# Kernel tuning notes

Measured on AMD Instinct MI355X. Metric: run time of the kernel, lower is better.

The kernel has to match this reference:

```python
import jax, jax.numpy as jnp
import numpy as np

NX, NY = 1024, 512
LX, LY = 0.26, 0.12
NU = 1e-4
U_INLET = 0.1
DX = LX / (NX - 1)
DY = LY / (NY - 1)
W_CONT, W_MOM, W_BC = 1.0, 0.1, 1.0


def _pad_x(f):
    # replicate pad along x axis (dim -2)
    return jnp.pad(f, ((0, 0), (0, 0), (1, 1), (0, 0)), mode='edge')


def _pad_y(f):
    return jnp.pad(f, ((0, 0), (0, 0), (0, 0), (1, 1)), mode='edge')


def ddx(f):
    p = _pad_x(f)
    return (p[:, :, 2:, :] - p[:, :, :-2, :]) / (2.0 * DX)


def ddy(f):
    p = _pad_y(f)
    return (p[:, :, :, 2:] - p[:, :, :, :-2]) / (2.0 * DY)


def d2dx2(f):
    p = _pad_x(f)
    return (p[:, :, 2:, :] - 2.0 * f + p[:, :, :-2, :]) / (DX * DX)


def d2dy2(f):
    p = _pad_y(f)
    return (p[:, :, :, 2:] - 2.0 * f + p[:, :, :, :-2]) / (DY * DY)


def masked_mean(x, mask):
    return (x * mask).sum() / jnp.maximum(mask.sum(), 1.0)


def region_masks(x_in):
    r = x_in[:, 1:2].astype(jnp.float32)  # [B,1,NX,NY] region codes
    fluid = (r > 0.5).astype(jnp.float32)
    obstacle = (r < 0.5).astype(jnp.float32)
    wall = ((r > 1.5) & (r < 2.5)).astype(jnp.float32)
    inlet = ((r > 2.5) & (r < 3.5)).astype(jnp.float32)
    outlet = (r > 3.5).astype(jnp.float32)
    noslip = ((obstacle + wall) > 0.5).astype(jnp.float32)
    # interior = fluid with zeroed 1-cell border
    border = jnp.zeros((NX, NY), jnp.float32).at[1:-1, 1:-1].set(1.0)
    interior = fluid * border
    return fluid, interior, noslip, inlet, outlet


def setup_inputs() -> dict:
    key = jax.random.key(0)
    k1, k2 = jax.random.split(key)
    y_hat = jax.random.normal(k1, (16, 3, NX, NY), dtype=jnp.float32)
    x_in = jax.random.randint(k2, (16, 2, NX, NY), 0, 5).astype(jnp.int32)
    return {'y_hat': y_hat, 'x_in': x_in}


def reference(y_hat, x_in):
    ux = y_hat[:, 0:1]
    uy = y_hat[:, 1:2]
    p = y_hat[:, 2:3]
    fluid, interior, noslip, inlet, outlet = region_masks(x_in)

    # continuity
    div = ddx(ux) + ddy(uy)
    l_cont = masked_mean(div ** 2, interior)

    # momentum
    res_x = ux * ddx(ux) + uy * ddy(ux) + ddx(p) - NU * (d2dx2(ux) + d2dy2(ux))
    res_y = ux * ddx(uy) + uy * ddy(uy) + ddy(p) - NU * (d2dx2(uy) + d2dy2(uy))
    l_mom = masked_mean(res_x ** 2, interior) + masked_mean(res_y ** 2, interior)

    # boundary (masked_mean already returns 0 for empty masks via denom clamp)
    l_bc = masked_mean(ux ** 2, noslip) + masked_mean(uy ** 2, noslip)
    l_bc = l_bc + masked_mean((ux - U_INLET) ** 2, inlet) + masked_mean(uy ** 2, inlet)
    l_bc = l_bc + masked_mean(ddx(ux) ** 2, outlet)

    total = W_CONT * l_cont + W_MOM * l_mom + W_BC * l_bc
    return jnp.stack([l_cont, l_mom, l_bc, total])
```

## Files before the change

kernel.cpp:

```cpp
#include <hip/hip_runtime.h>


namespace {
constexpr int NXc  = 1024;
constexpr int NYc  = 512;
constexpr int NXYc = NXc * NYc;
constexpr int NBc  = 16;
constexpr int NTHR = 256;
constexpr int NACC = 10;
constexpr int TR   = 4;
constexpr int NCH  = NXc / TR;
constexpr int NBLK = NBc * NCH;
constexpr int NXCD = 8;
constexpr int QX   = NBLK / NXCD;
}

__global__ __launch_bounds__(NTHR) void pil_main(const float* __restrict__ y,
                                                 const int* __restrict__ xin,
                                                 float* __restrict__ partial) {
  constexpr double DXd = 0.26 / 1023.0;
  constexpr double DYd = 0.12 / 511.0;
  const float INV2DX = (float)(1.0 / (2.0 * DXd));
  const float INV2DY = (float)(1.0 / (2.0 * DYd));
  const float INVDX2 = (float)(1.0 / (DXd * DXd));
  const float INVDY2 = (float)(1.0 / (DYd * DYd));
  constexpr float NU = 1e-4f;
  constexpr float U_INLET = 0.1f;

  __shared__ float lf[3][TR + 2][NYc];

  const int l   = threadIdx.x & 63;
  const int w   = threadIdx.x >> 6;
  const int swz = (blockIdx.x % NXCD) * QX + blockIdx.x / NXCD;
  const int b   = swz >> 8;
  const int i0  = (swz & (NCH - 1)) * TR;

  const float* __restrict__ ux = y + (size_t)b * 3 * NXYc;
  const float* __restrict__ uy = ux + NXYc;
  const float* __restrict__ pp = ux + 2 * NXYc;
  const int*   __restrict__ rp = xin + (size_t)(2 * b + 1) * NXYc;

#pragma unroll
  for (int k = 0; k < 9; ++k) {
    const int c  = k * 4 + w;
    const int f  = c / 12;
    const int cc = c % 12;
    const int rw = cc >> 1;
    const int h  = cc & 1;
    int gi = i0 - 1 + rw;
    gi = gi < 0 ? 0 : (gi > NXc - 1 ? NXc - 1 : gi);
    const float* base = (f == 0) ? ux : ((f == 1) ? uy : pp);
    const float* g = base + gi * NYc + h * 256 + l * 4;
    float* d = &lf[f][rw][h * 256];
    __builtin_amdgcn_global_load_lds(
        (const __attribute__((address_space(1))) void*)g,
        (__attribute__((address_space(3))) void*)d, 16, 0, 0);
  }

  const int i = i0 + w;
  const int jc = l << 3;
  const int4 R0 = *reinterpret_cast<const int4*>(rp + i * NYc + jc);
  const int4 R1 = *reinterpret_cast<const int4*>(rp + i * NYc + jc + 4);

  __syncthreads();

  const float4 Cxl = *reinterpret_cast<const float4*>(&lf[0][w + 1][jc]);
  const float4 Cxh = *reinterpret_cast<const float4*>(&lf[0][w + 1][jc + 4]);
  const float4 Cyl = *reinterpret_cast<const float4*>(&lf[1][w + 1][jc]);
  const float4 Cyh = *reinterpret_cast<const float4*>(&lf[1][w + 1][jc + 4]);
  const float4 Cpl = *reinterpret_cast<const float4*>(&lf[2][w + 1][jc]);
  const float4 Cph = *reinterpret_cast<const float4*>(&lf[2][w + 1][jc + 4]);
  const float4 Pxl = *reinterpret_cast<const float4*>(&lf[0][w][jc]);
  const float4 Pxh = *reinterpret_cast<const float4*>(&lf[0][w][jc + 4]);
  const float4 Pyl = *reinterpret_cast<const float4*>(&lf[1][w][jc]);
  const float4 Pyh = *reinterpret_cast<const float4*>(&lf[1][w][jc + 4]);
  const float4 Ppl = *reinterpret_cast<const float4*>(&lf[2][w][jc]);
  const float4 Pph = *reinterpret_cast<const float4*>(&lf[2][w][jc + 4]);
  const float4 Nxl = *reinterpret_cast<const float4*>(&lf[0][w + 2][jc]);
  const float4 Nxh = *reinterpret_cast<const float4*>(&lf[0][w + 2][jc + 4]);
  const float4 Nyl = *reinterpret_cast<const float4*>(&lf[1][w + 2][jc]);
  const float4 Nyh = *reinterpret_cast<const float4*>(&lf[1][w + 2][jc + 4]);
  const float4 Npl = *reinterpret_cast<const float4*>(&lf[2][w + 2][jc]);
  const float4 Nph = *reinterpret_cast<const float4*>(&lf[2][w + 2][jc + 4]);

  float a[NACC];
#pragma unroll
  for (int k = 0; k < NACC; ++k) a[k] = 0.f;

  const float cx[8]  = {Cxl.x, Cxl.y, Cxl.z, Cxl.w, Cxh.x, Cxh.y, Cxh.z, Cxh.w};
  const float cy_[8] = {Cyl.x, Cyl.y, Cyl.z, Cyl.w, Cyh.x, Cyh.y, Cyh.z, Cyh.w};
  const float cp_[8] = {Cpl.x, Cpl.y, Cpl.z, Cpl.w, Cph.x, Cph.y, Cph.z, Cph.w};
  const float pxA[8] = {Pxl.x, Pxl.y, Pxl.z, Pxl.w, Pxh.x, Pxh.y, Pxh.z, Pxh.w};
  const float pyA[8] = {Pyl.x, Pyl.y, Pyl.z, Pyl.w, Pyh.x, Pyh.y, Pyh.z, Pyh.w};
  const float ppA[8] = {Ppl.x, Ppl.y, Ppl.z, Ppl.w, Pph.x, Pph.y, Pph.z, Pph.w};
  const float nxA[8] = {Nxl.x, Nxl.y, Nxl.z, Nxl.w, Nxh.x, Nxh.y, Nxh.z, Nxh.w};
  const float nyA[8] = {Nyl.x, Nyl.y, Nyl.z, Nyl.w, Nyh.x, Nyh.y, Nyh.z, Nyh.w};
  const float npA[8] = {Npl.x, Npl.y, Npl.z, Npl.w, Nph.x, Nph.y, Nph.z, Nph.w};
  const int   rA[8]  = {R0.x, R0.y, R0.z, R0.w, R1.x, R1.y, R1.z, R1.w};

  float lxx = __shfl_up(cx[7], 1, 64);    if (l == 0)  lxx = cx[0];
  float rxx = __shfl_down(cx[0], 1, 64);  if (l == 63) rxx = cx[7];
  float lyy = __shfl_up(cy_[7], 1, 64);   if (l == 0)  lyy = cy_[0];
  float ryy = __shfl_down(cy_[0], 1, 64); if (l == 63) ryy = cy_[7];
  float lpp = __shfl_up(cp_[7], 1, 64);   if (l == 0)  lpp = cp_[0];
  float rpp = __shfl_down(cp_[0], 1, 64); if (l == 63) rpp = cp_[7];

  const bool irow = (i >= 1) & (i <= NXc - 2);

#pragma unroll
  for (int e = 0; e < 8; ++e) {
    const int   r    = rA[e];
    const float c_ux = cx[e], c_uy = cy_[e];
    const float uxm = (e == 0) ? lxx : cx[e - 1];
    const float uxp = (e == 7) ? rxx : cx[e + 1];
    const float uym = (e == 0) ? lyy : cy_[e - 1];
    const float uyp = (e == 7) ? ryy : cy_[e + 1];
    const float pm_ = (e == 0) ? lpp : cp_[e - 1];
    const float pq_ = (e == 7) ? rpp : cp_[e + 1];

    const float ddx_ux = (nxA[e] - pxA[e]) * INV2DX;
    const float ddy_ux = (uxp - uxm) * INV2DY;
    const float ddx_uy = (nyA[e] - pyA[e]) * INV2DX;
    const float ddy_uy = (uyp - uym) * INV2DY;

    const bool jedge = ((l == 0) & (e == 0)) | ((l == 63) & (e == 7));
    const bool interior = (r >= 1) & irow & (!jedge);
    if (interior) {
      const float dv    = ddx_ux + ddy_uy;
      const float d2xux = (nxA[e] - 2.f * c_ux + pxA[e]) * INVDX2;
      const float d2yux = (uxp - 2.f * c_ux + uxm) * INVDY2;
      const float d2xuy = (nyA[e] - 2.f * c_uy + pyA[e]) * INVDX2;
      const float d2yuy = (uyp - 2.f * c_uy + uym) * INVDY2;
      const float ddx_p = (npA[e] - ppA[e]) * INV2DX;
      const float ddy_p = (pq_ - pm_) * INV2DY;
      const float rxv = c_ux * ddx_ux + c_uy * ddy_ux + ddx_p - NU * (d2xux + d2yux);
      const float ryv = c_ux * ddx_uy + c_uy * ddy_uy + ddy_p - NU * (d2xuy + d2yuy);
      a[0] += dv * dv;
      a[1] += rxv * rxv;
      a[2] += ryv * ryv;
      a[3] += 1.f;
    }
    if ((r == 0) | (r == 2)) {
      a[4] += c_ux * c_ux + c_uy * c_uy;
      a[5] += 1.f;
    }
    if (r == 3) {
      const float d = c_ux - U_INLET;
      a[6] += d * d + c_uy * c_uy;
      a[7] += 1.f;
    }
    if (r == 4) {
      a[8] += ddx_ux * ddx_ux;
      a[9] += 1.f;
    }
  }

#pragma unroll
  for (int k = 0; k < NACC; ++k) {
    float v = a[k];
#pragma unroll
    for (int off = 32; off > 0; off >>= 1) v += __shfl_down(v, off, 64);
    a[k] = v;
  }

  __shared__ float sacc[NTHR / 64][NACC];
  if (l == 0) {
#pragma unroll
    for (int k = 0; k < NACC; ++k) sacc[w][k] = a[k];
  }
  __syncthreads();
  if (threadIdx.x < NACC) {
    float s = 0.f;
#pragma unroll
    for (int ww = 0; ww < NTHR / 64; ++ww) s += sacc[ww][threadIdx.x];
    partial[threadIdx.x * NBLK + blockIdx.x] = s;
  }
}

__global__ __launch_bounds__(256) void pil_finalize(const float* __restrict__ partial,
                                                    float* __restrict__ out) {
  __shared__ double sw[NACC][4];
  const int t = threadIdx.x;
  const int lane = t & 63, wave = t >> 6;
#pragma unroll
  for (int k = 0; k < NACC; ++k) {
    double v = 0.0;
    const float4* p4 = reinterpret_cast<const float4*>(partial + (size_t)k * NBLK);
    for (int bb = t; bb < NBLK / 4; bb += 256) {
      const float4 q = p4[bb];
      v += (double)q.x + (double)q.y + (double)q.z + (double)q.w;
    }
#pragma unroll
    for (int off = 32; off > 0; off >>= 1) v += __shfl_down(v, off, 64);
    if (lane == 0) sw[k][wave] = v;
  }
  __syncthreads();
  if (t == 0) {
    double acc[NACC];
#pragma unroll
    for (int k = 0; k < NACC; ++k) {
      double s = 0.0;
#pragma unroll
      for (int ww = 0; ww < 4; ++ww) s += sw[k][ww];
      acc[k] = s;
    }
    const double l_cont = acc[0] / fmax(acc[3], 1.0);
    const double l_mom  = (acc[1] + acc[2]) / fmax(acc[3], 1.0);
    const double l_bc   = acc[4] / fmax(acc[5], 1.0)
                        + acc[6] / fmax(acc[7], 1.0)
                        + acc[8] / fmax(acc[9], 1.0);
    const double total  = 1.0 * l_cont + 0.1 * l_mom + 1.0 * l_bc;
    out[0] = (float)l_cont;
    out[1] = (float)l_mom;
    out[2] = (float)l_bc;
    out[3] = (float)total;
  }
}

extern "C" void kernel_launch(void* const* d_in, const int* in_sizes, int n_in,
                              void* d_out, int out_size, void* d_ws, size_t ws_size,
                              hipStream_t stream) {
  const float* y   = (const float*)d_in[0];
  const int*   xin = (const int*)d_in[1];
  float* partial   = (float*)d_ws;

  pil_main<<<NBLK, NTHR, 0, stream>>>(y, xin, partial);
  pil_finalize<<<1, 256, 0, stream>>>(partial, (float*)d_out);
}
```

Measured before the change: 53.50 us.

## Double rows per block and load halo rows directly into registers

Each block now covers 8 rows with 512 threads instead of 4 rows with 256, which halves the number of blocks and lowers the share of redundant halo rows per block. The two halo rows are no longer staged in LDS. The first and last waves load them straight from global memory into registers, and the other waves read their neighbour rows from LDS. This cuts total global halo traffic and LDS footprint per row. The cost is larger blocks, divergent branches for the edge waves, and halo loads that are not covered by the async LDS copy.

```diff
diff --git a/kernel.cpp b/kernel.cpp
--- a/kernel.cpp
+++ b/kernel.cpp
@@ -6,9 +6,9 @@
 constexpr int NYc  = 512;
 constexpr int NXYc = NXc * NYc;
 constexpr int NBc  = 16;
-constexpr int NTHR = 256;
+constexpr int NTHR = 512;
 constexpr int NACC = 10;
-constexpr int TR   = 4;
+constexpr int TR   = 8;
 constexpr int NCH  = NXc / TR;
 constexpr int NBLK = NBc * NCH;
 constexpr int NXCD = 8;
@@ -27,12 +27,12 @@
   constexpr float NU = 1e-4f;
   constexpr float U_INLET = 0.1f;
 
-  __shared__ float lf[3][TR + 2][NYc];
+  __shared__ float lf[3][TR][NYc];
 
   const int l   = threadIdx.x & 63;
   const int w   = threadIdx.x >> 6;
   const int swz = (blockIdx.x % NXCD) * QX + blockIdx.x / NXCD;
-  const int b   = swz >> 8;
+  const int b   = swz >> 7;
   const int i0  = (swz & (NCH - 1)) * TR;
 
   const float* __restrict__ ux = y + (size_t)b * 3 * NXYc;
@@ -41,47 +41,69 @@
   const int*   __restrict__ rp = xin + (size_t)(2 * b + 1) * NXYc;
 
 #pragma unroll
-  for (int k = 0; k < 9; ++k) {
-    const int c  = k * 4 + w;
-    const int f  = c / 12;
-    const int cc = c % 12;
+  for (int k = 0; k < 6; ++k) {
+    const int c  = k * 8 + w;
+    const int f  = c >> 4;
+    const int cc = c & 15;
     const int rw = cc >> 1;
     const int h  = cc & 1;
-    int gi = i0 - 1 + rw;
-    gi = gi < 0 ? 0 : (gi > NXc - 1 ? NXc - 1 : gi);
     const float* base = (f == 0) ? ux : ((f == 1) ? uy : pp);
-    const float* g = base + gi * NYc + h * 256 + l * 4;
+    const float* g = base + (i0 + rw) * NYc + h * 256 + l * 4;
     float* d = &lf[f][rw][h * 256];
     __builtin_amdgcn_global_load_lds(
         (const __attribute__((address_space(1))) void*)g,
         (__attribute__((address_space(3))) void*)d, 16, 0, 0);
   }
 
-  const int i = i0 + w;
+  const int i  = i0 + w;
   const int jc = l << 3;
+
   const int4 R0 = *reinterpret_cast<const int4*>(rp + i * NYc + jc);
   const int4 R1 = *reinterpret_cast<const int4*>(rp + i * NYc + jc + 4);
 
+  float4 Hxl = {}, Hxh = {}, Hyl = {}, Hyh = {}, Hpl = {}, Hph = {};
+  if ((w == 0) | (w == 7)) {
+    const int hr = (w == 0) ? (i0 > 0 ? i0 - 1 : 0)
+                            : (i0 + TR < NXc ? i0 + TR : NXc - 1);
+    Hxl = *reinterpret_cast<const float4*>(ux + hr * NYc + jc);
+    Hxh = *reinterpret_cast<const float4*>(ux + hr * NYc + jc + 4);
+    Hyl = *reinterpret_cast<const float4*>(uy + hr * NYc + jc);
+    Hyh = *reinterpret_cast<const float4*>(uy + hr * NYc + jc + 4);
+    Hpl = *reinterpret_cast<const float4*>(pp + hr * NYc + jc);
+    Hph = *reinterpret_cast<const float4*>(pp + hr * NYc + jc + 4);
+  }
+
   __syncthreads();
 
-  const float4 Cxl = *reinterpret_cast<const float4*>(&lf[0][w + 1][jc]);
-  const float4 Cxh = *reinterpret_cast<const float4*>(&lf[0][w + 1][jc + 4]);
-  const float4 Cyl = *reinterpret_cast<const float4*>(&lf[1][w + 1][jc]);
-  const float4 Cyh = *reinterpret_cast<const float4*>(&lf[1][w + 1][jc + 4]);
-  const float4 Cpl = *reinterpret_cast<const float4*>(&lf[2][w + 1][jc]);
-  const float4 Cph = *reinterpret_cast<const float4*>(&lf[2][w + 1][jc + 4]);
-  const float4 Pxl = *reinterpret_cast<const float4*>(&lf[0][w][jc]);
-  const float4 Pxh = *reinterpret_cast<const float4*>(&lf[0][w][jc + 4]);
-  const float4 Pyl = *reinterpret_cast<const float4*>(&lf[1][w][jc]);
-  const float4 Pyh = *reinterpret_cast<const float4*>(&lf[1][w][jc + 4]);
-  const float4 Ppl = *reinterpret_cast<const float4*>(&lf[2][w][jc]);
-  const float4 Pph = *reinterpret_cast<const float4*>(&lf[2][w][jc + 4]);
-  const float4 Nxl = *reinterpret_cast<const float4*>(&lf[0][w + 2][jc]);
-  const float4 Nxh = *reinterpret_cast<const float4*>(&lf[0][w + 2][jc + 4]);
-  const float4 Nyl = *reinterpret_cast<const float4*>(&lf[1][w + 2][jc]);
-  const float4 Nyh = *reinterpret_cast<const float4*>(&lf[1][w + 2][jc + 4]);
-  const float4 Npl = *reinterpret_cast<const float4*>(&lf[2][w + 2][jc]);
-  const float4 Nph = *reinterpret_cast<const float4*>(&lf[2][w + 2][jc + 4]);
+  const float4 Cxl = *reinterpret_cast<const float4*>(&lf[0][w][jc]);
+  const float4 Cxh = *reinterpret_cast<const float4*>(&lf[0][w][jc + 4]);
+  const float4 Cyl = *reinterpret_cast<const float4*>(&lf[1][w][jc]);
+  const float4 Cyh = *reinterpret_cast<const float4*>(&lf[1][w][jc + 4]);
+  const float4 Cpl = *reinterpret_cast<const float4*>(&lf[2][w][jc]);
+  const float4 Cph = *reinterpret_cast<const float4*>(&lf[2][w][jc + 4]);
+
+  float4 Pxl, Pxh, Pyl, Pyh, Ppl, Pph;
+  if (w > 0) {
+    Pxl = *reinterpret_cast<const float4*>(&lf[0][w - 1][jc]);
+    Pxh = *reinterpret_cast<const float4*>(&lf[0][w - 1][jc + 4]);
+    Pyl = *reinterpret_cast<const float4*>(&lf[1][w - 1][jc]);
+    Pyh = *reinterpret_cast<const float4*>(&lf[1][w - 1][jc + 4]);
+    Ppl = *reinterpret_cast<const float4*>(&lf[2][w - 1][jc]);
+    Pph = *reinterpret_cast<const float4*>(&lf[2][w - 1][jc + 4]);
+  } else {
+    Pxl = Hxl; Pxh = Hxh; Pyl = Hyl; Pyh = Hyh; Ppl = Hpl; Pph = Hph;
+  }
+  float4 Nxl, Nxh, Nyl, Nyh, Npl, Nph;
+  if (w < TR - 1) {
+    Nxl = *reinterpret_cast<const float4*>(&lf[0][w + 1][jc]);
+    Nxh = *reinterpret_cast<const float4*>(&lf[0][w + 1][jc + 4]);
+    Nyl = *reinterpret_cast<const float4*>(&lf[1][w + 1][jc]);
+    Nyh = *reinterpret_cast<const float4*>(&lf[1][w + 1][jc + 4]);
+    Npl = *reinterpret_cast<const float4*>(&lf[2][w + 1][jc]);
+    Nph = *reinterpret_cast<const float4*>(&lf[2][w + 1][jc + 4]);
+  } else {
+    Nxl = Hxl; Nxh = Hxh; Nyl = Hyl; Nyh = Hyh; Npl = Hpl; Nph = Hph;
+  }
 
   float a[NACC];
 #pragma unroll
```

Result: faster. 45.23 us (-15.5%).
